# Kernel tuning notes

Measured on AMD Instinct MI355X. Metric: run time of the kernel, lower is better.

The kernel has to match this reference:

```python
import jax, jax.numpy as jnp
import numpy as np

# Geometry constants (from init_kwargs)
B, A, D = 16, 720, 1024          # batch, n_projections, n_detector_pixels
H, W = 512, 512                  # reconstruction volume
VOL_SPACING = 1.0                # pixel spacing (world units)
DET_SPACING = 1.0                # detector pixel spacing
ANG_RANGE = np.pi                # 180 deg parallel beam


def setup_inputs() -> dict:
    key = jax.random.key(0)
    sinogram = jax.random.normal(key, (B, A, D), dtype=jnp.float32)
    # Ramp (Ram-Lak) filter in FFT domain: |f| (real-valued), length D.
    freqs = np.fft.fftfreq(D)
    filt = jnp.asarray(2.0 * np.abs(freqs), dtype=jnp.float32)
    return {"sinogram": sinogram, "filt": filt}


def reference(sinogram, filt):
    # --- FFT ramp filtering along detector axis (norm='ortho') ---
    x = jnp.fft.fft(sinogram, axis=-1, norm="ortho")
    x = x * filt                                   # complex * real broadcast over [B,A,D]
    x = jnp.fft.ifft(x, axis=-1, norm="ortho").real.astype(jnp.float32)

    # --- Parallel-beam backprojection onto [H,W] grid ---
    angles = jnp.linspace(0.0, ANG_RANGE, A, endpoint=False, dtype=jnp.float32)
    cs, sn = jnp.cos(angles), jnp.sin(angles)      # [A]
    px = (jnp.arange(W, dtype=jnp.float32) - (W - 1) / 2.0) * VOL_SPACING  # [W]
    py = (jnp.arange(H, dtype=jnp.float32) - (H - 1) / 2.0) * VOL_SPACING  # [H]
    px = px[None, :]                               # [1,W]
    py = py[:, None]                               # [H,1]
    det_center = (D - 1) / 2.0

    sino_t = jnp.transpose(x, (1, 0, 2))           # [A,B,D]

    def step(acc, inp):
        c, s, proj = inp                           # proj: [B,D]
        # detector coordinate of each pixel's ray for this angle
        t = (px * c + py * s) / DET_SPACING + det_center   # [H,W]
        i0 = jnp.floor(t)
        w = t - i0                                 # linear-interp weight
        i0i = i0.astype(jnp.int32)
        i1i = i0i + 1
        valid = (i0i >= 0) & (i1i <= D - 1)
        i0c = jnp.clip(i0i, 0, D - 1)
        i1c = jnp.clip(i1i, 0, D - 1)
        v = proj[:, i0c] * (1.0 - w) + proj[:, i1c] * w    # [B,H,W]
        return acc + jnp.where(valid, v, 0.0), None

    img0 = jnp.zeros((B, H, W), dtype=jnp.float32)
    img, _ = jax.lax.scan(step, img0, (cs, sn, sino_t))
    # angular integration weight (d_theta = pi / A)
    return img * jnp.float32(ANG_RANGE / A)
```

## Files before the change

kernel.cpp:

```cpp
#include <hip/hip_runtime.h>
#include <hip/hip_fp16.h>
#include <math.h>

#define NB 16
#define NA 720
#define ND 1024
#define NH 512
#define NW 512

#define TW 64
#define TH 8
#define PXT 2
#define NBT 8
#define WINN 68
#define GROUP 16

typedef __fp16 h2vec __attribute__((ext_vector_type(2)));

__device__ __forceinline__ uint32_t pkrtz_u32(float a, float b) {
    union { h2vec h; uint32_t u; } v;
    v.h = __builtin_amdgcn_cvt_pkrtz(a, b);
    return v.u;
}
__device__ __forceinline__ __half2 u32_to_h2(uint32_t u) {
    union { uint32_t u; __half2 h; } v; v.u = u; return v.h;
}
__device__ __forceinline__ uint32_t h2_to_u32(__half2 h) {
    union { __half2 h; uint32_t u; } v; v.h = h; return v.u;
}

__global__ __launch_bounds__(768) void prep_kernel(float4* __restrict__ ptable) {
    const int a = threadIdx.x;
    const int pos = blockIdx.x;
    if (a >= NA) return;
    const float step = (float)(M_PI / (double)NA);
    float s, c;
    sincosf((float)a * step, &s, &c);
    const int bx = pos & 7, by = pos >> 3;
    const float x0 = (float)(bx * TW) - 255.5f;
    const float x1 = x0 + (float)(TW - 1);
    const float y0 = (float)(by * TH) - 255.5f;
    const float tmin = 511.5f + fminf(x0 * c, x1 * c) + y0 * s;
    const int base = (int)floorf(tmin) - 1;
    ptable[pos * NA + a] = make_float4(c, s, 511.5f - (float)base,
                                       __int_as_float(a * ND + base));
}

#define SZ(i) ((i) ^ (((i) >> 4) & 15))

__device__ __forceinline__ float2 cmul(float2 w, float2 v) {
    return make_float2(w.x * v.x - w.y * v.y, w.x * v.y + w.y * v.x);
}
__device__ __forceinline__ float2 cmulc(float2 w, float2 v) {
    return make_float2(w.x * v.x + w.y * v.y, w.x * v.y - w.y * v.x);
}

__global__ __launch_bounds__(256) void filter_kernel(const float* __restrict__ sino,
                                                     const float* __restrict__ filt,
                                                     uint32_t* __restrict__ packed) {
    __shared__ float2 bufA[ND];
    __shared__ float2 bufB[ND];
    __shared__ float2 tw4[768];

    const int tid = threadIdx.x;
    const int a = blockIdx.x;
    const int p = blockIdx.y;
    const float* __restrict__ xa = sino + ((size_t)(2 * p) * NA + a) * ND;
    const float* __restrict__ xb = xa + (size_t)NA * ND;
    uint32_t* __restrict__ yo = packed + ((size_t)(2 * p) * NA + a) * ND;

    #pragma unroll
    for (int i = 0; i < ND; i += 256)
        bufA[SZ(i + tid)] = make_float2(xa[i + tid], xb[i + tid]);
    #pragma unroll
    for (int i = 0; i < 768; i += 256) {
        int m = i + tid;
        float ang = (float)(-2.0 * M_PI / (double)ND) * (float)m;
        float s, c;
        sincosf(ang, &s, &c);
        tw4[SZ(m)] = make_float2(c, s);
    }
    __syncthreads();

    float2* src = bufA;
    float2* dst = bufB;

    for (int Ns = 1; Ns < ND; Ns <<= 2) {
        const int j = tid;
        const int m = j & (Ns - 1);
        const int tstep = (ND / 4) / Ns;
        float2 u0 = src[SZ(j)];
        float2 x1 = src[SZ(j + 256)];
        float2 x2 = src[SZ(j + 512)];
        float2 x3 = src[SZ(j + 768)];
        float2 w1 = tw4[SZ(m * tstep)];
        float2 w2 = tw4[SZ(2 * m * tstep)];
        float2 w3 = tw4[SZ(3 * m * tstep)];
        float2 u1 = cmul(w1, x1), u2 = cmul(w2, x2), u3 = cmul(w3, x3);
        float2 A  = make_float2(u0.x + u2.x, u0.y + u2.y);
        float2 Bb = make_float2(u0.x - u2.x, u0.y - u2.y);
        float2 C  = make_float2(u1.x + u3.x, u1.y + u3.y);
        float2 D  = make_float2(u1.x - u3.x, u1.y - u3.y);
        const int d = ((j & ~(Ns - 1)) << 2) + m;
        dst[SZ(d)]          = make_float2(A.x + C.x, A.y + C.y);
        dst[SZ(d + Ns)]     = make_float2(Bb.x + D.y, Bb.y - D.x);
        dst[SZ(d + 2 * Ns)] = make_float2(A.x - C.x, A.y - C.y);
        dst[SZ(d + 3 * Ns)] = make_float2(Bb.x - D.y, Bb.y + D.x);
        __syncthreads();
        float2* tmp = src; src = dst; dst = tmp;
    }

    const float SCALE = 1.0f / (float)ND;
    #pragma unroll
    for (int i = 0; i < ND; i += 256) {
        float f = filt[i + tid] * SCALE;
        src[SZ(i + tid)].x *= f;
        src[SZ(i + tid)].y *= f;
    }
    __syncthreads();

    for (int Ns = 1; Ns < ND; Ns <<= 2) {
        const int j = tid;
        const int m = j & (Ns - 1);
        const int tstep = (ND / 4) / Ns;
        float2 u0 = src[SZ(j)];
        float2 x1 = src[SZ(j + 256)];
        float2 x2 = src[SZ(j + 512)];
        float2 x3 = src[SZ(j + 768)];
        float2 w1 = tw4[SZ(m * tstep)];
        float2 w2 = tw4[SZ(2 * m * tstep)];
        float2 w3 = tw4[SZ(3 * m * tstep)];
        float2 u1 = cmulc(w1, x1), u2 = cmulc(w2, x2), u3 = cmulc(w3, x3);
        float2 A  = make_float2(u0.x + u2.x, u0.y + u2.y);
        float2 Bb = make_float2(u0.x - u2.x, u0.y - u2.y);
        float2 C  = make_float2(u1.x + u3.x, u1.y + u3.y);
        float2 D  = make_float2(u1.x - u3.x, u1.y - u3.y);
        const int d = ((j & ~(Ns - 1)) << 2) + m;
        dst[SZ(d)]          = make_float2(A.x + C.x, A.y + C.y);
        dst[SZ(d + Ns)]     = make_float2(Bb.x - D.y, Bb.y + D.x);
        dst[SZ(d + 2 * Ns)] = make_float2(A.x - C.x, A.y - C.y);
        dst[SZ(d + 3 * Ns)] = make_float2(Bb.x + D.y, Bb.y - D.x);
        __syncthreads();
        float2* tmp = src; src = dst; dst = tmp;
    }

    #pragma unroll
    for (int i = 0; i < ND; i += 256) {
        float2 v = src[SZ(i + tid)];
        yo[i + tid] = pkrtz_u32(v.x, v.y);
    }
}

__global__ __launch_bounds__(256, 4) void backproj_kernel(const uint32_t* __restrict__ packed,
                                                          const float4* __restrict__ ptable,
                                                          float* __restrict__ img) {
    __shared__ __align__(16) uint4 win[2][4][WINN];

    const int tid = threadIdx.x;
    const int bx = blockIdx.x, by = blockIdx.y, bz = blockIdx.z;

    const float4* __restrict__ pt = ptable + (size_t)((by << 3) + bx) * NA;

    const bool stg = tid < 2 * WINN;
    const int sg   = (tid >= WINN) ? 1 : 0;
    const int si   = tid - sg * WINN;
    const uint32_t* __restrict__ sbA =
        packed + (size_t)(2 * (4 * bz + 2 * sg)) * NA * ND + si;
    const uint32_t* __restrict__ sbB = sbA + (size_t)2 * NA * ND;
    uint4* const wptr = &win[sg][0][si];

    const int lane = tid & 63;
    const int wid  = tid >> 6;
    const int tx0  = (wid << 4) + (lane & 7);
    const int ty   = lane >> 3;
    const float px  = (float)(bx * TW + tx0) - 255.5f;
    const float pyf = (float)(by * TH + ty)  - 255.5f;

    float accf[8][PXT];
    __half2 hacc01[PXT], hacc23[PXT], hacc45[PXT], hacc67[PXT];
    #pragma unroll
    for (int k = 0; k < PXT; k++) {
        #pragma unroll
        for (int b = 0; b < 8; b++) accf[b][k] = 0.0f;
        hacc01[k] = u32_to_h2(0u); hacc23[k] = u32_to_h2(0u);
        hacc45[k] = u32_to_h2(0u); hacc67[k] = u32_to_h2(0u);
    }

    auto stage_load = [&](float4 P, uint2& wA, uint2& wB) {
        const int off = __float_as_int(P.w);
        const uint32_t* pa = sbA + off;
        const uint32_t* pb = sbB + off;
        wA = make_uint2(pa[0], pa[1]);
        wB = make_uint2(pb[0], pb[1]);
    };
    auto stage_write = [&](int ph, uint2 wA, uint2 wB) {
        wptr[ph * WINN] = make_uint4(
            wA.x, h2_to_u32(__hsub2(u32_to_h2(wA.y), u32_to_h2(wA.x))),
            wB.x, h2_to_u32(__hsub2(u32_to_h2(wB.y), u32_to_h2(wB.x))));
    };
    auto compute = [&](float4 P, int ph) {
        const float tb = fmaf(px, P.x, fmaf(pyf, P.y, P.z));
        #pragma unroll
        for (int k = 0; k < PXT; k++) {
            float t  = fmaf((float)(8 * k), P.x, tb);
            int   i0 = (int)t;
#if __has_builtin(__builtin_amdgcn_fractf)
            float w  = __builtin_amdgcn_fractf(t);
#else
            float w  = t - (float)i0;
#endif
            __half2 wh2 = u32_to_h2(pkrtz_u32(w, w));
            const uint4 qA = win[0][ph][i0];
            const uint4 qB = win[1][ph][i0];
            hacc01[k] = __hfma2(wh2, u32_to_h2(qA.y), __hadd2(hacc01[k], u32_to_h2(qA.x)));
            hacc23[k] = __hfma2(wh2, u32_to_h2(qA.w), __hadd2(hacc23[k], u32_to_h2(qA.z)));
            hacc45[k] = __hfma2(wh2, u32_to_h2(qB.y), __hadd2(hacc45[k], u32_to_h2(qB.x)));
            hacc67[k] = __hfma2(wh2, u32_to_h2(qB.w), __hadd2(hacc67[k], u32_to_h2(qB.z)));
        }
    };

    uint2 h2A = make_uint2(0, 0), h2B = make_uint2(0, 0);
    uint2 h3A = make_uint2(0, 0), h3B = make_uint2(0, 0);
    if (stg) {
        uint2 wA, wB;
        stage_load(pt[0], wA, wB);  stage_write(0, wA, wB);
        stage_load(pt[1], wA, wB);  stage_write(1, wA, wB);
        stage_load(pt[2], h2A, h2B);
        stage_load(pt[3], h3A, h3B);
    }
    __syncthreads();

    for (int g = 0; g < NA; g += GROUP) {
        #pragma unroll 1
        for (int it = 0; it < GROUP / 4; it++) {
            const int a = g + it * 4;
            const float4 P0 = pt[a],     P1 = pt[a + 1];
            const float4 P2 = pt[a + 2], P3 = pt[a + 3];
            const float4 P4 = pt[min(a + 4, NA - 1)], P5 = pt[min(a + 5, NA - 1)];
            const float4 P6 = pt[min(a + 6, NA - 1)], P7 = pt[min(a + 7, NA - 1)];

            uint2 l4A = make_uint2(0, 0), l4B = make_uint2(0, 0);
            uint2 l5A = make_uint2(0, 0), l5B = make_uint2(0, 0);
            if (stg) {
                stage_load(P4, l4A, l4B);
                stage_load(P5, l5A, l5B);
                stage_write(2, h2A, h2B);
                stage_write(3, h3A, h3B);
            }
            compute(P0, 0);
            compute(P1, 1);
            __syncthreads();

            uint2 l6A = make_uint2(0, 0), l6B = make_uint2(0, 0);
            uint2 l7A = make_uint2(0, 0), l7B = make_uint2(0, 0);
            if (stg) {
                stage_load(P6, l6A, l6B);
                stage_load(P7, l7A, l7B);
                stage_write(0, l4A, l4B);
                stage_write(1, l5A, l5B);
            }
            compute(P2, 2);
            compute(P3, 3);
            h2A = l6A; h2B = l6B; h3A = l7A; h3B = l7B;
            __syncthreads();
        }
        #pragma unroll
        for (int k = 0; k < PXT; k++) {
            float2 v01 = __half22float2(hacc01[k]);
            float2 v23 = __half22float2(hacc23[k]);
            float2 v45 = __half22float2(hacc45[k]);
            float2 v67 = __half22float2(hacc67[k]);
            accf[0][k] += v01.x; accf[1][k] += v01.y;
            accf[2][k] += v23.x; accf[3][k] += v23.y;
            accf[4][k] += v45.x; accf[5][k] += v45.y;
            accf[6][k] += v67.x; accf[7][k] += v67.y;
            hacc01[k] = u32_to_h2(0u); hacc23[k] = u32_to_h2(0u);
            hacc45[k] = u32_to_h2(0u); hacc67[k] = u32_to_h2(0u);
        }
    }

    const float SCALE = (float)(M_PI / (double)NA);
    const size_t bstride = (size_t)NH * NW;
    size_t o0 = (((size_t)(bz * NBT) * NH) + (by * TH + ty)) * NW + (bx * TW + tx0);
    #pragma unroll
    for (int k = 0; k < PXT; k++) {
        #pragma unroll
        for (int b = 0; b < 8; b++)
            img[o0 + (size_t)(8 * k) + (size_t)b * bstride] = accf[b][k] * SCALE;
    }
}

extern "C" void kernel_launch(void* const* d_in, const int* in_sizes, int n_in,
                              void* d_out, int out_size, void* d_ws, size_t ws_size,
                              hipStream_t stream) {
    const float* sino = (const float*)d_in[0];
    const float* filt = (const float*)d_in[1];
    float* out = (float*)d_out;

    const size_t pack_bytes = (size_t)NB * NA * ND * sizeof(uint32_t);
    const size_t ptab_bytes = (size_t)512 * NA * sizeof(float4);
    uint32_t* packed;
    float4* ptable;
    if (ws_size >= pack_bytes + ptab_bytes) {
        packed = (uint32_t*)d_ws;
        ptable = (float4*)((char*)d_ws + pack_bytes);
    } else {
        packed = (uint32_t*)d_in[0];
        ptable = (float4*)d_ws;
    }

    prep_kernel<<<dim3(512), dim3(768), 0, stream>>>(ptable);
    filter_kernel<<<dim3(NA, NB / 2), dim3(256), 0, stream>>>(sino, filt, packed);
    backproj_kernel<<<dim3(NW / TW, NH / TH, NB / NBT), dim3(256), 0, stream>>>(packed, ptable, out);
}
```

Baseline: 377.1 us.

## Serve half the batches from global gather buffer instead of LDS window

The filter kernel also writes an interleaved (value, next-value) half2 gather buffer for batches 4-7 and 12-15. Backprojection stages only batches 0-3 of each group into LDS and reads the other four straight from global or L2 with one 16-byte load per pixel per angle. The aim is to halve LDS staging work and LDS footprint, at the cost of extra global writes in the filter pass, extra workspace, and scattered global loads inside the inner loop. The old LDS-only kernel is kept as a fallback when the workspace is too small.

```diff
diff --git a/kernel.cpp b/kernel.cpp
--- a/kernel.cpp
+++ b/kernel.cpp
@@ -57,7 +57,8 @@
 
 __global__ __launch_bounds__(256) void filter_kernel(const float* __restrict__ sino,
                                                      const float* __restrict__ filt,
-                                                     uint32_t* __restrict__ packed) {
+                                                     uint32_t* __restrict__ packed,
+                                                     uint4* __restrict__ gbuf) {
     __shared__ float2 bufA[ND];
     __shared__ float2 bufB[ND];
     __shared__ float2 tw4[768];
@@ -144,16 +145,167 @@
         float2* tmp = src; src = dst; dst = tmp;
     }
 
+    const int duo = (p == 2 || p == 3) ? 0 : (p == 6 || p == 7) ? 1 : -1;
     #pragma unroll
     for (int i = 0; i < ND; i += 256) {
-        float2 v = src[SZ(i + tid)];
-        yo[i + tid] = pkrtz_u32(v.x, v.y);
+        const int idx = i + tid;
+        float2 v = src[SZ(idx)];
+        uint32_t u = pkrtz_u32(v.x, v.y);
+        yo[idx] = u;
+        if (gbuf != nullptr && duo >= 0) {
+            float2 vn = src[SZ(min(idx + 1, ND - 1))];
+            uint32_t un = pkrtz_u32(vn.x, vn.y);
+            char* e = (char*)(gbuf + ((size_t)duo * NA + a) * ND + idx)
+                      + ((p & 1) ? 8 : 0);
+            *(uint2*)e = make_uint2(u, un);
+        }
     }
 }
 
 __global__ __launch_bounds__(256, 4) void backproj_kernel(const uint32_t* __restrict__ packed,
+                                                          const uint4* __restrict__ gbuf,
                                                           const float4* __restrict__ ptable,
                                                           float* __restrict__ img) {
+    __shared__ __align__(16) uint4 win[4][WINN];
+
+    const int tid = threadIdx.x;
+    const int bx = blockIdx.x, by = blockIdx.y, bz = blockIdx.z;
+
+    const float4* __restrict__ pt = ptable + (size_t)((by << 3) + bx) * NA;
+    const uint4* __restrict__ Gb = gbuf + (size_t)bz * NA * ND;
+
+    const bool stg = tid < WINN;
+    const uint32_t* __restrict__ sbA =
+        packed + (size_t)(2 * (4 * bz)) * NA * ND + tid;
+    const uint32_t* __restrict__ sbB = sbA + (size_t)2 * NA * ND;
+    uint4* const wptr = &win[0][tid < WINN ? tid : 0];
+
+    const int lane = tid & 63;
+    const int wid  = tid >> 6;
+    const int tx0  = (wid << 4) + (lane & 7);
+    const int ty   = lane >> 3;
+    const float px  = (float)(bx * TW + tx0) - 255.5f;
+    const float pyf = (float)(by * TH + ty)  - 255.5f;
+
+    float accf[8][PXT];
+    __half2 hacc01[PXT], hacc23[PXT], hacc45[PXT], hacc67[PXT];
+    #pragma unroll
+    for (int k = 0; k < PXT; k++) {
+        #pragma unroll
+        for (int b = 0; b < 8; b++) accf[b][k] = 0.0f;
+        hacc01[k] = u32_to_h2(0u); hacc23[k] = u32_to_h2(0u);
+        hacc45[k] = u32_to_h2(0u); hacc67[k] = u32_to_h2(0u);
+    }
+
+    auto stage_load = [&](float4 P, uint2& wA, uint2& wB) {
+        const int off = __float_as_int(P.w);
+        const uint32_t* pa = sbA + off;
+        const uint32_t* pb = sbB + off;
+        wA = make_uint2(pa[0], pa[1]);
+        wB = make_uint2(pb[0], pb[1]);
+    };
+    auto stage_write = [&](int ph, uint2 wA, uint2 wB) {
+        wptr[ph * WINN] = make_uint4(
+            wA.x, h2_to_u32(__hsub2(u32_to_h2(wA.y), u32_to_h2(wA.x))),
+            wB.x, h2_to_u32(__hsub2(u32_to_h2(wB.y), u32_to_h2(wB.x))));
+    };
+    auto compute = [&](float4 P, int ph) {
+        const float tb = fmaf(px, P.x, fmaf(pyf, P.y, P.z));
+        #pragma unroll
+        for (int k = 0; k < PXT; k++) {
+            float t  = fmaf((float)(8 * k), P.x, tb);
+            int   i0 = (int)t;
+#if __has_builtin(__builtin_amdgcn_fractf)
+            float w  = __builtin_amdgcn_fractf(t);
+#else
+            float w  = t - (float)i0;
+#endif
+            __half2 wh2 = u32_to_h2(pkrtz_u32(w, w));
+            const uint4 qA = win[ph][i0];
+            const uint4 gv = Gb[__float_as_int(P.w) + i0];
+            hacc01[k] = __hfma2(wh2, u32_to_h2(qA.y), __hadd2(hacc01[k], u32_to_h2(qA.x)));
+            hacc23[k] = __hfma2(wh2, u32_to_h2(qA.w), __hadd2(hacc23[k], u32_to_h2(qA.z)));
+            __half2 F2 = u32_to_h2(gv.x), F2n = u32_to_h2(gv.y);
+            hacc45[k] = __hfma2(wh2, __hsub2(F2n, F2), __hadd2(hacc45[k], F2));
+            __half2 F3 = u32_to_h2(gv.z), F3n = u32_to_h2(gv.w);
+            hacc67[k] = __hfma2(wh2, __hsub2(F3n, F3), __hadd2(hacc67[k], F3));
+        }
+    };
+
+    uint2 h2A = make_uint2(0, 0), h2B = make_uint2(0, 0);
+    uint2 h3A = make_uint2(0, 0), h3B = make_uint2(0, 0);
+    if (stg) {
+        uint2 wA, wB;
+        stage_load(pt[0], wA, wB);  stage_write(0, wA, wB);
+        stage_load(pt[1], wA, wB);  stage_write(1, wA, wB);
+        stage_load(pt[2], h2A, h2B);
+        stage_load(pt[3], h3A, h3B);
+    }
+    __syncthreads();
+
+    for (int g = 0; g < NA; g += GROUP) {
+        #pragma unroll 1
+        for (int it = 0; it < GROUP / 4; it++) {
+            const int a = g + it * 4;
+            const float4 P0 = pt[a],     P1 = pt[a + 1];
+            const float4 P2 = pt[a + 2], P3 = pt[a + 3];
+            const float4 P4 = pt[min(a + 4, NA - 1)], P5 = pt[min(a + 5, NA - 1)];
+            const float4 P6 = pt[min(a + 6, NA - 1)], P7 = pt[min(a + 7, NA - 1)];
+
+            uint2 l4A = make_uint2(0, 0), l4B = make_uint2(0, 0);
+            uint2 l5A = make_uint2(0, 0), l5B = make_uint2(0, 0);
+            if (stg) {
+                stage_load(P4, l4A, l4B);
+                stage_load(P5, l5A, l5B);
+                stage_write(2, h2A, h2B);
+                stage_write(3, h3A, h3B);
+            }
+            compute(P0, 0);
+            compute(P1, 1);
+            __syncthreads();
+
+            uint2 l6A = make_uint2(0, 0), l6B = make_uint2(0, 0);
+            uint2 l7A = make_uint2(0, 0), l7B = make_uint2(0, 0);
+            if (stg) {
+                stage_load(P6, l6A, l6B);
+                stage_load(P7, l7A, l7B);
+                stage_write(0, l4A, l4B);
+                stage_write(1, l5A, l5B);
+            }
+            compute(P2, 2);
+            compute(P3, 3);
+            h2A = l6A; h2B = l6B; h3A = l7A; h3B = l7B;
+            __syncthreads();
+        }
+        #pragma unroll
+        for (int k = 0; k < PXT; k++) {
+            float2 v01 = __half22float2(hacc01[k]);
+            float2 v23 = __half22float2(hacc23[k]);
+            float2 v45 = __half22float2(hacc45[k]);
+            float2 v67 = __half22float2(hacc67[k]);
+            accf[0][k] += v01.x; accf[1][k] += v01.y;
+            accf[2][k] += v23.x; accf[3][k] += v23.y;
+            accf[4][k] += v45.x; accf[5][k] += v45.y;
+            accf[6][k] += v67.x; accf[7][k] += v67.y;
+            hacc01[k] = u32_to_h2(0u); hacc23[k] = u32_to_h2(0u);
+            hacc45[k] = u32_to_h2(0u); hacc67[k] = u32_to_h2(0u);
+        }
+    }
+
+    const float SCALE = (float)(M_PI / (double)NA);
+    const size_t bstride = (size_t)NH * NW;
+    size_t o0 = (((size_t)(bz * NBT) * NH) + (by * TH + ty)) * NW + (bx * TW + tx0);
+    #pragma unroll
+    for (int k = 0; k < PXT; k++) {
+        #pragma unroll
+        for (int b = 0; b < 8; b++)
+            img[o0 + (size_t)(8 * k) + (size_t)b * bstride] = accf[b][k] * SCALE;
+    }
+}
+
+__global__ __launch_bounds__(256, 4) void backproj_kernel_lds(const uint32_t* __restrict__ packed,
+                                                              const float4* __restrict__ ptable,
+                                                              float* __restrict__ img) {
     __shared__ __align__(16) uint4 win[2][4][WINN];
 
     const int tid = threadIdx.x;
@@ -188,10 +340,8 @@
 
     auto stage_load = [&](float4 P, uint2& wA, uint2& wB) {
         const int off = __float_as_int(P.w);
-        const uint32_t* pa = sbA + off;
-        const uint32_t* pb = sbB + off;
-        wA = make_uint2(pa[0], pa[1]);
-        wB = make_uint2(pb[0], pb[1]);
+        wA = make_uint2(sbA[off], sbA[off + 1]);
+        wB = make_uint2(sbB[off], sbB[off + 1]);
     };
     auto stage_write = [&](int ph, uint2 wA, uint2 wB) {
         wptr[ph * WINN] = make_uint4(
@@ -298,10 +448,18 @@
     float* out = (float*)d_out;
 
     const size_t pack_bytes = (size_t)NB * NA * ND * sizeof(uint32_t);
+    const size_t g_bytes    = (size_t)2 * NA * ND * sizeof(uint4);
     const size_t ptab_bytes = (size_t)512 * NA * sizeof(float4);
+
     uint32_t* packed;
+    uint4* gbuf = nullptr;
     float4* ptable;
-    if (ws_size >= pack_bytes + ptab_bytes) {
+
+    if (ws_size >= pack_bytes + g_bytes + ptab_bytes) {
+        packed = (uint32_t*)d_ws;
+        gbuf   = (uint4*)((char*)d_ws + pack_bytes);
+        ptable = (float4*)((char*)d_ws + pack_bytes + g_bytes);
+    } else if (ws_size >= pack_bytes + ptab_bytes) {
         packed = (uint32_t*)d_ws;
         ptable = (float4*)((char*)d_ws + pack_bytes);
     } else {
@@ -310,6 +468,10 @@
     }
 
     prep_kernel<<<dim3(512), dim3(768), 0, stream>>>(ptable);
-    filter_kernel<<<dim3(NA, NB / 2), dim3(256), 0, stream>>>(sino, filt, packed);
-    backproj_kernel<<<dim3(NW / TW, NH / TH, NB / NBT), dim3(256), 0, stream>>>(packed, ptable, out);
-}
+    filter_kernel<<<dim3(NA, NB / 2), dim3(256), 0, stream>>>(sino, filt, packed, gbuf);
+    if (gbuf != nullptr) {
+        backproj_kernel<<<dim3(NW / TW, NH / TH, NB / NBT), dim3(256), 0, stream>>>(packed, gbuf, ptable, out);
+    } else {
+        backproj_kernel_lds<<<dim3(NW / TW, NH / TH, NB / NBT), dim3(256), 0, stream>>>(packed, ptable, out);
+    }
+}
```

New measurement: 432.3 us. 1.15x slower.

## Double-buffer backprojection window to one barrier per four angles; precompute FFT twiddles

Applied to the files above, without the earlier changes.

The backprojection staging window grows to eight phases and alternates between two halves of four angles. This cuts the barriers from two per four angles to one, and the global loads for the next group now overlap the compute on the current group. The fp16-to-fp32 flush moves into the loop every sixteen angles. FFT twiddles are computed once by an extra prep block and loaded from global memory instead of running sincosf in every filter block. The cost is a larger shared-memory footprint in the backprojection kernel, which may lower occupancy, and a raw lgkmcnt-wait barrier that relies on correct memory ordering.

```diff
diff --git a/kernel.cpp b/kernel.cpp
--- a/kernel.cpp
+++ b/kernel.cpp
@@ -13,7 +13,6 @@
 #define PXT 2
 #define NBT 8
 #define WINN 68
-#define GROUP 16
 
 typedef __fp16 h2vec __attribute__((ext_vector_type(2)));
 
@@ -29,9 +28,17 @@
     union { __half2 h; uint32_t u; } v; v.h = h; return v.u;
 }
 
-__global__ __launch_bounds__(768) void prep_kernel(float4* __restrict__ ptable) {
+__global__ __launch_bounds__(768) void prep_kernel(float4* __restrict__ ptable,
+                                                   float2* __restrict__ twg) {
     const int a = threadIdx.x;
     const int pos = blockIdx.x;
+    if (pos == 512) {
+        float ang = (float)(-2.0 * M_PI / 1024.0) * (float)a;
+        float s, c;
+        sincosf(ang, &s, &c);
+        twg[a] = make_float2(c, s);
+        return;
+    }
     if (a >= NA) return;
     const float step = (float)(M_PI / (double)NA);
     float s, c;
@@ -57,6 +64,7 @@
 
 __global__ __launch_bounds__(256) void filter_kernel(const float* __restrict__ sino,
                                                      const float* __restrict__ filt,
+                                                     const float2* __restrict__ twg,
                                                      uint32_t* __restrict__ packed) {
     __shared__ float2 bufA[ND];
     __shared__ float2 bufB[ND];
@@ -75,10 +83,7 @@
     #pragma unroll
     for (int i = 0; i < 768; i += 256) {
         int m = i + tid;
-        float ang = (float)(-2.0 * M_PI / (double)ND) * (float)m;
-        float s, c;
-        sincosf(ang, &s, &c);
-        tw4[SZ(m)] = make_float2(c, s);
+        tw4[SZ(m)] = twg[m];
     }
     __syncthreads();
 
@@ -154,7 +159,7 @@
 __global__ __launch_bounds__(256, 4) void backproj_kernel(const uint32_t* __restrict__ packed,
                                                           const float4* __restrict__ ptable,
                                                           float* __restrict__ img) {
-    __shared__ __align__(16) uint4 win[2][4][WINN];
+    __shared__ __align__(16) uint4 win[2][8][WINN];
 
     const int tid = threadIdx.x;
     const int bx = blockIdx.x, by = blockIdx.y, bz = blockIdx.z;
@@ -185,6 +190,11 @@
         hacc01[k] = u32_to_h2(0u); hacc23[k] = u32_to_h2(0u);
         hacc45[k] = u32_to_h2(0u); hacc67[k] = u32_to_h2(0u);
     }
+
+    auto bar = []() {
+        asm volatile("s_waitcnt lgkmcnt(0)" ::: "memory");
+        __builtin_amdgcn_s_barrier();
+    };
 
     auto stage_load = [&](float4 P, uint2& wA, uint2& wB) {
         const int off = __float_as_int(P.w);
@@ -198,7 +208,7 @@
             wA.x, h2_to_u32(__hsub2(u32_to_h2(wA.y), u32_to_h2(wA.x))),
             wB.x, h2_to_u32(__hsub2(u32_to_h2(wB.y), u32_to_h2(wB.x))));
     };
-    auto compute = [&](float4 P, int ph) {
+    auto consume = [&](float4 P, int ph) {
         const float tb = fmaf(px, P.x, fmaf(pyf, P.y, P.z));
         #pragma unroll
         for (int k = 0; k < PXT; k++) {
@@ -219,64 +229,63 @@
         }
     };
 
+    uint2 h0A = make_uint2(0, 0), h0B = make_uint2(0, 0);
+    uint2 h1A = make_uint2(0, 0), h1B = make_uint2(0, 0);
     uint2 h2A = make_uint2(0, 0), h2B = make_uint2(0, 0);
     uint2 h3A = make_uint2(0, 0), h3B = make_uint2(0, 0);
+
     if (stg) {
         uint2 wA, wB;
         stage_load(pt[0], wA, wB);  stage_write(0, wA, wB);
         stage_load(pt[1], wA, wB);  stage_write(1, wA, wB);
-        stage_load(pt[2], h2A, h2B);
-        stage_load(pt[3], h3A, h3B);
-    }
-    __syncthreads();
-
-    for (int g = 0; g < NA; g += GROUP) {
-        #pragma unroll 1
-        for (int it = 0; it < GROUP / 4; it++) {
-            const int a = g + it * 4;
-            const float4 P0 = pt[a],     P1 = pt[a + 1];
-            const float4 P2 = pt[a + 2], P3 = pt[a + 3];
-            const float4 P4 = pt[min(a + 4, NA - 1)], P5 = pt[min(a + 5, NA - 1)];
-            const float4 P6 = pt[min(a + 6, NA - 1)], P7 = pt[min(a + 7, NA - 1)];
-
-            uint2 l4A = make_uint2(0, 0), l4B = make_uint2(0, 0);
-            uint2 l5A = make_uint2(0, 0), l5B = make_uint2(0, 0);
-            if (stg) {
-                stage_load(P4, l4A, l4B);
-                stage_load(P5, l5A, l5B);
-                stage_write(2, h2A, h2B);
-                stage_write(3, h3A, h3B);
+        stage_load(pt[2], wA, wB);  stage_write(2, wA, wB);
+        stage_load(pt[3], wA, wB);  stage_write(3, wA, wB);
+        stage_load(pt[4], h0A, h0B);
+        stage_load(pt[5], h1A, h1B);
+        stage_load(pt[6], h2A, h2B);
+        stage_load(pt[7], h3A, h3B);
+    }
+    bar();
+
+    #pragma unroll 1
+    for (int r = 0; r < NA / 4; ++r) {
+        const int a = 4 * r;
+        const int cb = (r & 1) * 4;
+        const int ob = cb ^ 4;
+        const float4 P0 = pt[a],     P1 = pt[a + 1];
+        const float4 P2 = pt[a + 2], P3 = pt[a + 3];
+
+        if (stg) {
+            stage_write(ob + 0, h0A, h0B);
+            stage_write(ob + 1, h1A, h1B);
+            stage_write(ob + 2, h2A, h2B);
+            stage_write(ob + 3, h3A, h3B);
+            stage_load(pt[min(a + 8,  NA - 1)], h0A, h0B);
+            stage_load(pt[min(a + 9,  NA - 1)], h1A, h1B);
+            stage_load(pt[min(a + 10, NA - 1)], h2A, h2B);
+            stage_load(pt[min(a + 11, NA - 1)], h3A, h3B);
+        }
+        consume(P0, cb + 0);
+        consume(P1, cb + 1);
+        consume(P2, cb + 2);
+        consume(P3, cb + 3);
+
+        if ((r & 3) == 3) {
+            #pragma unroll
+            for (int k = 0; k < PXT; k++) {
+                float2 v01 = __half22float2(hacc01[k]);
+                float2 v23 = __half22float2(hacc23[k]);
+                float2 v45 = __half22float2(hacc45[k]);
+                float2 v67 = __half22float2(hacc67[k]);
+                accf[0][k] += v01.x; accf[1][k] += v01.y;
+                accf[2][k] += v23.x; accf[3][k] += v23.y;
+                accf[4][k] += v45.x; accf[5][k] += v45.y;
+                accf[6][k] += v67.x; accf[7][k] += v67.y;
+                hacc01[k] = u32_to_h2(0u); hacc23[k] = u32_to_h2(0u);
+                hacc45[k] = u32_to_h2(0u); hacc67[k] = u32_to_h2(0u);
             }
-            compute(P0, 0);
-            compute(P1, 1);
-            __syncthreads();
-
-            uint2 l6A = make_uint2(0, 0), l6B = make_uint2(0, 0);
-            uint2 l7A = make_uint2(0, 0), l7B = make_uint2(0, 0);
-            if (stg) {
-                stage_load(P6, l6A, l6B);
-                stage_load(P7, l7A, l7B);
-                stage_write(0, l4A, l4B);
-                stage_write(1, l5A, l5B);
-            }
-            compute(P2, 2);
-            compute(P3, 3);
-            h2A = l6A; h2B = l6B; h3A = l7A; h3B = l7B;
-            __syncthreads();
         }
-        #pragma unroll
-        for (int k = 0; k < PXT; k++) {
-            float2 v01 = __half22float2(hacc01[k]);
-            float2 v23 = __half22float2(hacc23[k]);
-            float2 v45 = __half22float2(hacc45[k]);
-            float2 v67 = __half22float2(hacc67[k]);
-            accf[0][k] += v01.x; accf[1][k] += v01.y;
-            accf[2][k] += v23.x; accf[3][k] += v23.y;
-            accf[4][k] += v45.x; accf[5][k] += v45.y;
-            accf[6][k] += v67.x; accf[7][k] += v67.y;
-            hacc01[k] = u32_to_h2(0u); hacc23[k] = u32_to_h2(0u);
-            hacc45[k] = u32_to_h2(0u); hacc67[k] = u32_to_h2(0u);
-        }
+        bar();
     }
 
     const float SCALE = (float)(M_PI / (double)NA);
@@ -299,17 +308,23 @@
 
     const size_t pack_bytes = (size_t)NB * NA * ND * sizeof(uint32_t);
     const size_t ptab_bytes = (size_t)512 * NA * sizeof(float4);
+    const size_t twg_bytes  = (size_t)768 * sizeof(float2);
+
     uint32_t* packed;
     float4* ptable;
-    if (ws_size >= pack_bytes + ptab_bytes) {
+    float2* twg;
+
+    if (ws_size >= pack_bytes + ptab_bytes + twg_bytes) {
         packed = (uint32_t*)d_ws;
         ptable = (float4*)((char*)d_ws + pack_bytes);
+        twg    = (float2*)((char*)d_ws + pack_bytes + ptab_bytes);
     } else {
         packed = (uint32_t*)d_in[0];
         ptable = (float4*)d_ws;
-    }
-
-    prep_kernel<<<dim3(512), dim3(768), 0, stream>>>(ptable);
-    filter_kernel<<<dim3(NA, NB / 2), dim3(256), 0, stream>>>(sino, filt, packed);
+        twg    = (float2*)((char*)d_ws + ptab_bytes);
+    }
+
+    prep_kernel<<<dim3(513), dim3(768), 0, stream>>>(ptable, twg);
+    filter_kernel<<<dim3(NA, NB / 2), dim3(256), 0, stream>>>(sino, filt, twg, packed);
     backproj_kernel<<<dim3(NW / TW, NH / TH, NB / NBT), dim3(256), 0, stream>>>(packed, ptable, out);
 }
```

Measured after the change: 366.0 us. 2.9% less time.
